# Optimization experiments

Hardware: AMD Instinct MI355X
Metric: run time of the kernel (lower is better)

The kernel has to match this reference:

```python
import jax, jax.numpy as jnp
import numpy as np

B, S, H, D = 4, 2048, 8, 64  # batch, seq, heads, per-head dim (dim=64)
EPS = 1e-5


def _layernorm(h, g, b):
    m = jnp.mean(h, axis=-1, keepdims=True)
    v = jnp.mean(jnp.square(h - m), axis=-1, keepdims=True)
    return (h - m) * jax.lax.rsqrt(v + EPS) * g + b


def setup_inputs() -> dict:
    key = jax.random.key(0)
    ks = jax.random.split(key, 12)
    s = 1.0 / np.sqrt(D)
    return {
        "x": jax.random.normal(ks[0], (B, S, H, D), dtype=jnp.float32),
        "ln1_g": jnp.ones((D,), jnp.float32),
        "ln1_b": jnp.zeros((D,), jnp.float32),
        "Wp": jax.random.normal(ks[1], (D, 3 * D), jnp.float32) * s,
        "bp": jnp.zeros((3 * D,), jnp.float32),
        "ln2_g": jnp.ones((D,), jnp.float32),
        "ln2_b": jnp.zeros((D,), jnp.float32),
        "W1": jax.random.normal(ks[2], (D, 4 * D), jnp.float32) * s,
        "b1": jnp.zeros((4 * D,), jnp.float32),
        "W2": jax.random.normal(ks[3], (4 * D, D), jnp.float32) * (1.0 / np.sqrt(4 * D)),
        "b2": jnp.zeros((D,), jnp.float32),
    }


def reference(x, ln1_g, ln1_b, Wp, bp, ln2_g, ln2_b, W1, b1, W2, b2):
    # x: [B, S, H, D]
    h = _layernorm(x, ln1_g, ln1_b)
    qkv = h @ Wp + bp                       # [B,S,H,3D]  (dropout = identity, eval)
    q, k, v = jnp.split(qkv, 3, axis=-1)
    q = q.transpose(0, 2, 1, 3)             # [B,H,S,D]
    k = k.transpose(0, 2, 1, 3)
    v = v.transpose(0, 2, 1, 3)
    sim = jnp.einsum('bhqd,bhkd->bhqk', q, k)   # no sqrt(d) scaling (faithful)
    attn = jax.nn.softmax(sim, axis=-1)
    out = jnp.einsum('bhqk,bhkd->bhqd', attn, v).transpose(0, 2, 1, 3)  # [B,S,H,D]
    out = _layernorm(out, ln2_g, ln2_b)
    out = jax.nn.gelu(out @ W1 + b1, approximate=False) @ W2 + b2
    return out + x
```

## Files before the change

### kernel.cpp

```cpp
#include <hip/hip_runtime.h>
#include <hip/hip_bf16.h>
#include <math.h>

#define BB 4
#define SS 2048
#define HH 8
#define DD 64
#define EPSV 1e-5f

typedef __attribute__((ext_vector_type(8))) short short8;
typedef __attribute__((ext_vector_type(4))) float f32x4;
typedef unsigned short ushort_t;
#define MFMA16 __builtin_amdgcn_mfma_f32_16x16x32_bf16

__device__ inline unsigned short f2bf(float f) {
    unsigned u = __builtin_bit_cast(unsigned, f);
    unsigned r = (u + 0x7fffu + ((u >> 16) & 1u)) >> 16;
    return (unsigned short)r;
}
__device__ inline float bf2f(unsigned short h) {
    unsigned u = ((unsigned)h) << 16;
    return __builtin_bit_cast(float, u);
}
__device__ inline unsigned pkbf(float a, float b) {
    __hip_bfloat162 h2 = __float22bfloat162_rn(make_float2(a, b));
    unsigned u;
    __builtin_memcpy(&u, &h2, 4);
    return u;
}

__global__ __launch_bounds__(256) void k0_prep(
    const float* __restrict__ Wp, const float* __restrict__ W1,
    const float* __restrict__ W2, ushort_t* __restrict__ WpTh,
    ushort_t* __restrict__ WpTl, ushort_t* __restrict__ W1T,
    ushort_t* __restrict__ W2T)
{
    int gid = blockIdx.x * 256 + threadIdx.x;
    if (gid < 12288) {
        int n = gid >> 6, k = gid & 63;
        float w = Wp[k * 192 + n];
        ushort_t hi = f2bf(w);
        WpTh[gid] = hi;
        WpTl[gid] = f2bf(w - bf2f(hi));
    }
    {
        int n = gid >> 6, k = gid & 63;
        W1T[gid] = f2bf(W1[k * 256 + n]);
    }
    {
        int n = gid >> 8, k = gid & 255;
        W2T[gid] = f2bf(W2[k * 64 + n]);
    }
}

__global__ __launch_bounds__(256) void k1_ln_qkv(
    const float* __restrict__ x, const float* __restrict__ g1, const float* __restrict__ b1v,
    const ushort_t* __restrict__ WpTh, const ushort_t* __restrict__ WpTl,
    const float* __restrict__ bp,
    float* __restrict__ qws, ushort_t* __restrict__ khws, ushort_t* __restrict__ vtws)
{
    __shared__ __align__(16) ushort_t Hh[64 * 72];
    __shared__ __align__(16) ushort_t Hl[64 * 72];
    __shared__ __align__(16) ushort_t Vt[64 * 72];

    const int tid = threadIdx.x;
    const int wv  = tid >> 6;
    const int lane = tid & 63;
    const int l15 = lane & 15;
    const int g   = lane >> 4;
    const int bh  = blockIdx.x & 31;
    const int sc  = blockIdx.x >> 5;
    const int b   = bh >> 3, hh = bh & 7;
    const int s0  = sc * 64;

    short8 bqh[2], bql[2], bkh[2], bkl[2], bvh[2];
    #pragma unroll
    for (int kh = 0; kh < 2; ++kh) {
        int koff = kh * 32 + g * 8;
        bqh[kh] = *(const short8*)(WpTh + (wv * 16 + l15) * 64 + koff);
        bql[kh] = *(const short8*)(WpTl + (wv * 16 + l15) * 64 + koff);
        bkh[kh] = *(const short8*)(WpTh + (64 + wv * 16 + l15) * 64 + koff);
        bkl[kh] = *(const short8*)(WpTl + (64 + wv * 16 + l15) * 64 + koff);
        bvh[kh] = *(const short8*)(WpTh + (128 + wv * 16 + l15) * 64 + koff);
    }
    const float biasq = bp[wv * 16 + l15];
    const float biask = bp[64 + wv * 16 + l15];
    const float biasv = bp[128 + wv * 16 + l15];

    {
        const int srow = s0 + wv * 16 + l15;
        const float* xr = x + ((size_t)(b * 2048 + srow) * 8 + hh) * 64;
        float hvv[16];
        #pragma unroll
        for (int kh = 0; kh < 2; ++kh) {
            float4 p0 = *(const float4*)(xr + kh * 32 + g * 8);
            float4 p1 = *(const float4*)(xr + kh * 32 + g * 8 + 4);
            hvv[kh*8+0]=p0.x; hvv[kh*8+1]=p0.y; hvv[kh*8+2]=p0.z; hvv[kh*8+3]=p0.w;
            hvv[kh*8+4]=p1.x; hvv[kh*8+5]=p1.y; hvv[kh*8+6]=p1.z; hvv[kh*8+7]=p1.w;
        }
        float s1 = 0.0f;
        #pragma unroll
        for (int i = 0; i < 16; ++i) s1 += hvv[i];
        s1 += __shfl_xor(s1, 16, 64);
        s1 += __shfl_xor(s1, 32, 64);
        float mean = s1 * (1.0f / 64.0f);
        float s2 = 0.0f;
        #pragma unroll
        for (int i = 0; i < 16; ++i) { float d = hvv[i] - mean; s2 += d * d; }
        s2 += __shfl_xor(s2, 16, 64);
        s2 += __shfl_xor(s2, 32, 64);
        float rstd = rsqrtf(s2 * (1.0f / 64.0f) + EPSV);

        #pragma unroll
        for (int kh = 0; kh < 2; ++kh) {
            ushort_t hi[8]; unsigned lo2[4];
            float hf[8];
            #pragma unroll
            for (int j = 0; j < 8; ++j) {
                int dI = kh * 32 + g * 8 + j;
                hf[j] = (hvv[kh*8+j] - mean) * rstd * g1[dI] + b1v[dI];
                hi[j] = f2bf(hf[j]);
            }
            uint4 HHv;
            HHv.x = (unsigned)hi[0] | ((unsigned)hi[1] << 16);
            HHv.y = (unsigned)hi[2] | ((unsigned)hi[3] << 16);
            HHv.z = (unsigned)hi[4] | ((unsigned)hi[5] << 16);
            HHv.w = (unsigned)hi[6] | ((unsigned)hi[7] << 16);
            #pragma unroll
            for (int j = 0; j < 4; ++j)
                lo2[j] = pkbf(hf[2*j] - bf2f(hi[2*j]), hf[2*j+1] - bf2f(hi[2*j+1]));
            uint4 HLv; HLv.x = lo2[0]; HLv.y = lo2[1]; HLv.z = lo2[2]; HLv.w = lo2[3];
            int off = (wv * 16 + l15) * 72 + kh * 32 + g * 8;
            *(uint4*)(&Hh[off]) = HHv;
            *(uint4*)(&Hl[off]) = HLv;
        }
    }
    __syncthreads();

    #pragma unroll
    for (int mt = 0; mt < 4; ++mt) {
        short8 ah[2], al[2];
        int abase = (mt * 16 + l15) * 72 + g * 8;
        ah[0] = *(const short8*)(&Hh[abase]);
        ah[1] = *(const short8*)(&Hh[abase + 32]);
        al[0] = *(const short8*)(&Hl[abase]);
        al[1] = *(const short8*)(&Hl[abase + 32]);

        f32x4 aq = (f32x4){0.f,0.f,0.f,0.f};
        f32x4 ak = (f32x4){0.f,0.f,0.f,0.f};
        f32x4 av = (f32x4){0.f,0.f,0.f,0.f};
        #pragma unroll
        for (int kh = 0; kh < 2; ++kh) {
            aq = MFMA16(ah[kh], bqh[kh], aq, 0, 0, 0);
            aq = MFMA16(al[kh], bqh[kh], aq, 0, 0, 0);
            aq = MFMA16(ah[kh], bql[kh], aq, 0, 0, 0);
            ak = MFMA16(ah[kh], bkh[kh], ak, 0, 0, 0);
            ak = MFMA16(al[kh], bkh[kh], ak, 0, 0, 0);
            ak = MFMA16(ah[kh], bkl[kh], ak, 0, 0, 0);
            av = MFMA16(ah[kh], bvh[kh], av, 0, 0, 0);
        }

        size_t base = ((size_t)bh * 2048 + s0 + mt * 16 + 4 * g) * 64 + wv * 16 + l15;
        #pragma unroll
        for (int r = 0; r < 4; ++r) {
            qws[base + (size_t)r * 64] = aq[r] + biasq;
            khws[base + (size_t)r * 64] = f2bf(ak[r] + biask);
        }
        uint2 vvp;
        vvp.x = pkbf(av[0] + biasv, av[1] + biasv);
        vvp.y = pkbf(av[2] + biasv, av[3] + biasv);
        *(uint2*)(&Vt[(wv * 16 + l15) * 72 + mt * 16 + 4 * g]) = vvp;
    }
    __syncthreads();

    #pragma unroll
    for (int p = 0; p < 2; ++p) {
        int slot = tid + 256 * p;
        int dd = slot >> 3, cc = slot & 7;
        *(uint4*)(vtws + ((size_t)bh * 64 + dd) * 2048 + s0 + cc * 8) =
            *(const uint4*)(&Vt[dd * 72 + cc * 8]);
    }
}

#define LROW 72
#define NKT 32

__global__ __launch_bounds__(256, 2) void k2_attn(
    const float* __restrict__ qws, const ushort_t* __restrict__ khws,
    const ushort_t* __restrict__ vtws, float* __restrict__ ows)
{
    __shared__ __align__(16) ushort_t KhL[2][64 * LROW];
    __shared__ __align__(16) ushort_t VtL[2][64 * LROW];
    __shared__ __align__(16) ushort_t PL[128 * LROW];

    const int tid  = threadIdx.x;
    const int w    = tid >> 6;
    const int lane = tid & 63;
    const int l15  = lane & 15;
    const int g    = lane >> 4;
    const int bh   = blockIdx.x & 31;
    const int qb0  = (blockIdx.x >> 5) * 128;

    const float LOG2E = 1.4426950408889634f;
    short8 qh[2][2], ql[2][2];
    #pragma unroll
    for (int sub = 0; sub < 2; ++sub) {
        const float* qp = qws + ((size_t)bh * SS + qb0 + w * 32 + sub * 16 + l15) * 64;
        #pragma unroll
        for (int kh = 0; kh < 2; ++kh) {
            const float* p = qp + 32 * kh + 8 * g;
            #pragma unroll
            for (int j = 0; j < 8; ++j) {
                float f = p[j] * LOG2E;
                ushort_t hi = f2bf(f);
                qh[sub][kh][j] = (short)hi;
                ql[sub][kh][j] = (short)f2bf(f - bf2f(hi));
            }
        }
    }

    float lrow[2] = {0.0f, 0.0f};
    f32x4 oacc[2][4];
    #pragma unroll
    for (int sub = 0; sub < 2; ++sub)
        #pragma unroll
        for (int dt = 0; dt < 4; ++dt) oacc[sub][dt] = (f32x4){0.f, 0.f, 0.f, 0.f};

    const size_t kbase = (size_t)bh * SS * 64;
    const size_t vbase = (size_t)bh * 64 * 2048;

    uint4 kb[2], vb[2];
    #pragma unroll
    for (int rr = 0; rr < 2; ++rr) {
        int slot = tid + 256 * rr;
        int row = slot >> 3, seg = slot & 7;
        kb[rr] = *(const uint4*)(khws + kbase + (size_t)row * 64 + seg * 8);
        vb[rr] = *(const uint4*)(vtws + vbase + (size_t)row * 2048 + seg * 8);
    }
    #pragma unroll
    for (int rr = 0; rr < 2; ++rr) {
        int slot = tid + 256 * rr;
        int row = slot >> 3, seg = slot & 7;
        *(uint4*)(&KhL[0][row * LROW + seg * 8]) = kb[rr];
        *(uint4*)(&VtL[0][row * LROW + seg * 8]) = vb[rr];
    }

    for (int kt = 0; kt < NKT; ++kt) {
        __syncthreads();
        const int cur = kt & 1;

        if (kt < NKT - 1) {
            #pragma unroll
            for (int rr = 0; rr < 2; ++rr) {
                int slot = tid + 256 * rr;
                int row = slot >> 3, seg = slot & 7;
                kb[rr] = *(const uint4*)(khws + kbase + (size_t)((kt + 1) * 64 + row) * 64 + seg * 8);
                vb[rr] = *(const uint4*)(vtws + vbase + (size_t)row * 2048 + (kt + 1) * 64 + seg * 8);
            }
        }

        #pragma unroll
        for (int nf = 0; nf < 4; ++nf) {
            f32x4 aA = (f32x4){0.f, 0.f, 0.f, 0.f};
            f32x4 aB = (f32x4){0.f, 0.f, 0.f, 0.f};
            #pragma unroll
            for (int kh = 0; kh < 2; ++kh) {
                short8 kah = *(const short8*)(&KhL[cur][(nf * 16 + l15) * LROW + 32 * kh + 8 * g]);
                aA = MFMA16(kah, qh[0][kh], aA, 0, 0, 0);
                aA = MFMA16(kah, ql[0][kh], aA, 0, 0, 0);
                aB = MFMA16(kah, qh[1][kh], aB, 0, 0, 0);
                aB = MFMA16(kah, ql[1][kh], aB, 0, 0, 0);
            }
            {
                float p0 = __builtin_amdgcn_exp2f(aA[0]);
                float p1 = __builtin_amdgcn_exp2f(aA[1]);
                float p2 = __builtin_amdgcn_exp2f(aA[2]);
                float p3 = __builtin_amdgcn_exp2f(aA[3]);
                lrow[0] += (p0 + p1) + (p2 + p3);
                uint2 pk; pk.x = pkbf(p0, p1); pk.y = pkbf(p2, p3);
                *(uint2*)(&PL[(w * 32 + l15) * LROW + nf * 16 + 4 * g]) = pk;
            }
            {
                float p0 = __builtin_amdgcn_exp2f(aB[0]);
                float p1 = __builtin_amdgcn_exp2f(aB[1]);
                float p2 = __builtin_amdgcn_exp2f(aB[2]);
                float p3 = __builtin_amdgcn_exp2f(aB[3]);
                lrow[1] += (p0 + p1) + (p2 + p3);
                uint2 pk; pk.x = pkbf(p0, p1); pk.y = pkbf(p2, p3);
                *(uint2*)(&PL[(w * 32 + 16 + l15) * LROW + nf * 16 + 4 * g]) = pk;
            }
        }

        #pragma unroll
        for (int k2i = 0; k2i < 2; ++k2i) {
            short8 paA = *(const short8*)(&PL[(w * 32 + l15) * LROW + k2i * 32 + 8 * g]);
            short8 paB = *(const short8*)(&PL[(w * 32 + 16 + l15) * LROW + k2i * 32 + 8 * g]);
            #pragma unroll
            for (int dt = 0; dt < 4; ++dt) {
                short8 vbf = *(const short8*)(&VtL[cur][(16 * dt + l15) * LROW + k2i * 32 + 8 * g]);
                oacc[0][dt] = MFMA16(paA, vbf, oacc[0][dt], 0, 0, 0);
                oacc[1][dt] = MFMA16(paB, vbf, oacc[1][dt], 0, 0, 0);
            }
        }

        if (kt < NKT - 1) {
            #pragma unroll
            for (int rr = 0; rr < 2; ++rr) {
                int slot = tid + 256 * rr;
                int row = slot >> 3, seg = slot & 7;
                *(uint4*)(&KhL[cur ^ 1][row * LROW + seg * 8]) = kb[rr];
                *(uint4*)(&VtL[cur ^ 1][row * LROW + seg * 8]) = vb[rr];
            }
        }
    }

    #pragma unroll
    for (int sub = 0; sub < 2; ++sub) {
        float l = lrow[sub];
        l += __shfl_xor(l, 16, 64);
        l += __shfl_xor(l, 32, 64);
        float il = 1.0f / l;
        #pragma unroll
        for (int r = 0; r < 4; ++r) {
            float ilr = __shfl(il, 4 * g + r, 64);
            int row = qb0 + w * 32 + sub * 16 + 4 * g + r;
            #pragma unroll
            for (int dt = 0; dt < 4; ++dt)
                ows[((size_t)bh * SS + row) * 64 + dt * 16 + l15] = oacc[sub][dt][r] * ilr;
        }
    }
}

#define ITERS 4

__global__ __launch_bounds__(256) void k3_ln_mlp(
    const float* __restrict__ ows, const float* __restrict__ x,
    const float* __restrict__ g2, const float* __restrict__ b2v,
    const ushort_t* __restrict__ W1T, const float* __restrict__ b1m,
    const ushort_t* __restrict__ W2T, const float* __restrict__ b2o,
    float* __restrict__ out)
{
    __shared__ __align__(16) ushort_t Hs[16 * 264];
    __shared__ __align__(16) float Rs[4 * 16 * 72];

    const int tid  = threadIdx.x;
    const int wv   = tid >> 6;
    const int lane = tid & 63;
    const int l15  = lane & 15;
    const int g    = lane >> 4;

    short8 w1f[4][2], w2f[4][2];
    float  b1r[4][4];
    #pragma unroll
    for (int t = 0; t < 4; ++t) {
        #pragma unroll
        for (int kh = 0; kh < 2; ++kh) {
            w1f[t][kh] = *(const short8*)(W1T + (wv * 64 + t * 16 + l15) * 64 + kh * 32 + g * 8);
            w2f[t][kh] = *(const short8*)(W2T + (t * 16 + l15) * 256 + wv * 64 + kh * 32 + g * 8);
        }
        #pragma unroll
        for (int r = 0; r < 4; ++r)
            b1r[t][r] = b1m[wv * 64 + t * 16 + 4 * g + r];
    }

    for (int it = 0; it < ITERS; ++it) {
        const int r0 = (blockIdx.x * ITERS + it) * 16;

        const float* orow = ows + (size_t)(r0 + l15) * 64;
        float hvv[16];
        #pragma unroll
        for (int kh = 0; kh < 2; ++kh) {
            float4 p0 = *(const float4*)(orow + kh * 32 + g * 8);
            float4 p1 = *(const float4*)(orow + kh * 32 + g * 8 + 4);
            hvv[kh*8+0]=p0.x; hvv[kh*8+1]=p0.y; hvv[kh*8+2]=p0.z; hvv[kh*8+3]=p0.w;
            hvv[kh*8+4]=p1.x; hvv[kh*8+5]=p1.y; hvv[kh*8+6]=p1.z; hvv[kh*8+7]=p1.w;
        }
        float s1 = 0.0f;
        #pragma unroll
        for (int i = 0; i < 16; ++i) s1 += hvv[i];
        s1 += __shfl_xor(s1, 16, 64);
        s1 += __shfl_xor(s1, 32, 64);
        float mean = s1 * (1.0f / 64.0f);
        float s2 = 0.0f;
        #pragma unroll
        for (int i = 0; i < 16; ++i) { float d = hvv[i] - mean; s2 += d * d; }
        s2 += __shfl_xor(s2, 16, 64);
        s2 += __shfl_xor(s2, 32, 64);
        float rstd = rsqrtf(s2 * (1.0f / 64.0f) + EPSV);

        short8 h2f[2];
        #pragma unroll
        for (int kh = 0; kh < 2; ++kh) {
            float4 ga = *(const float4*)(g2 + kh * 32 + g * 8);
            float4 gb = *(const float4*)(g2 + kh * 32 + g * 8 + 4);
            float4 ba = *(const float4*)(b2v + kh * 32 + g * 8);
            float4 bb = *(const float4*)(b2v + kh * 32 + g * 8 + 4);
            float gg[8] = {ga.x,ga.y,ga.z,ga.w,gb.x,gb.y,gb.z,gb.w};
            float bv[8] = {ba.x,ba.y,ba.z,ba.w,bb.x,bb.y,bb.z,bb.w};
            #pragma unroll
            for (int j = 0; j < 8; ++j)
                h2f[kh][j] = (short)f2bf((hvv[kh*8+j] - mean) * rstd * gg[j] + bv[j]);
        }

        #pragma unroll
        for (int t = 0; t < 4; ++t) {
            f32x4 acc = (f32x4){0.f, 0.f, 0.f, 0.f};
            acc = MFMA16(w1f[t][0], h2f[0], acc, 0, 0, 0);
            acc = MFMA16(w1f[t][1], h2f[1], acc, 0, 0, 0);
            float ge[4];
            #pragma unroll
            for (int r = 0; r < 4; ++r) {
                float v = acc[r] + b1r[t][r];
                ge[r] = 0.5f * v * (1.0f + erff(v * 0.70710678118654752f));
            }
            uint2 pk;
            pk.x = pkbf(ge[0], ge[1]);
            pk.y = pkbf(ge[2], ge[3]);
            *(uint2*)(&Hs[l15 * 264 + wv * 64 + t * 16 + 4 * g]) = pk;
        }

        short8 ha[2];
        ha[0] = *(const short8*)(&Hs[l15 * 264 + wv * 64 + g * 8]);
        ha[1] = *(const short8*)(&Hs[l15 * 264 + wv * 64 + 32 + g * 8]);
        #pragma unroll
        for (int t = 0; t < 4; ++t) {
            f32x4 a2 = (f32x4){0.f, 0.f, 0.f, 0.f};
            a2 = MFMA16(ha[0], w2f[t][0], a2, 0, 0, 0);
            a2 = MFMA16(ha[1], w2f[t][1], a2, 0, 0, 0);
            #pragma unroll
            for (int r = 0; r < 4; ++r)
                Rs[wv * 1152 + (4 * g + r) * 72 + t * 16 + l15] = a2[r];
        }
        __syncthreads();

        {
            int m = tid >> 4, d4 = tid & 15;
            const float* rp = Rs + m * 72 + d4 * 4;
            f32x4 v0 = *(const f32x4*)(rp);
            f32x4 v1 = *(const f32x4*)(rp + 1152);
            f32x4 v2 = *(const f32x4*)(rp + 2304);
            f32x4 v3 = *(const f32x4*)(rp + 3456);
            f32x4 sum = v0 + v1 + v2 + v3;
            int r = r0 + m;
            int bq = r >> 14, hq = (r >> 11) & 7, sq = r & 2047;
            size_t oidx = ((size_t)(bq * 2048 + sq) * 8 + hq) * 64 + d4 * 4;
            float4 xv = *(const float4*)(x + oidx);
            float4 bo = *(const float4*)(b2o + d4 * 4);
            float4 res = make_float4(sum[0] + xv.x + bo.x, sum[1] + xv.y + bo.y,
                                     sum[2] + xv.z + bo.z, sum[3] + xv.w + bo.w);
            *(float4*)(out + oidx) = res;
        }
        __syncthreads();
    }
}

extern "C" void kernel_launch(void* const* d_in, const int* in_sizes, int n_in,
                              void* d_out, int out_size, void* d_ws, size_t ws_size,
                              hipStream_t stream) {
    const float* x     = (const float*)d_in[0];
    const float* ln1_g = (const float*)d_in[1];
    const float* ln1_b = (const float*)d_in[2];
    const float* Wp    = (const float*)d_in[3];
    const float* bp    = (const float*)d_in[4];
    const float* ln2_g = (const float*)d_in[5];
    const float* ln2_b = (const float*)d_in[6];
    const float* W1    = (const float*)d_in[7];
    const float* b1    = (const float*)d_in[8];
    const float* W2    = (const float*)d_in[9];
    const float* b2    = (const float*)d_in[10];
    float* out = (float*)d_out;

    float* ws  = (float*)d_ws;
    float* qws = ws;
    float* ows = ws + 4194304;
    ushort_t* khws = (ushort_t*)(ws + 8388608);
    ushort_t* vtws = khws + 4194304;
    ushort_t* WpTh = vtws + 4194304;
    ushort_t* WpTl = WpTh + 12288;
    ushort_t* W1T  = WpTl + 12288;
    ushort_t* W2T  = W1T + 16384;

    k0_prep<<<dim3(64), dim3(256), 0, stream>>>(Wp, W1, W2, WpTh, WpTl, W1T, W2T);
    k1_ln_qkv<<<dim3(1024), dim3(256), 0, stream>>>(
        x, ln1_g, ln1_b, WpTh, WpTl, bp, qws, khws, vtws);
    k2_attn<<<dim3(512), dim3(256), 0, stream>>>(qws, khws, vtws, ows);
    k3_ln_mlp<<<dim3(BB * HH * SS / 16 / ITERS), dim3(256), 0, stream>>>(
        ows, x, ln2_g, ln2_b, W1T, b1, W2T, b2, out);
}
```

Measured before the change: 187.6 us.

## Give each attention wave 64 query rows and precompute split-bf16 Q in QKV kernel

```diff
diff --git a/kernel.cpp b/kernel.cpp
--- a/kernel.cpp
+++ b/kernel.cpp
@@ -57,7 +57,8 @@
     const float* __restrict__ x, const float* __restrict__ g1, const float* __restrict__ b1v,
     const ushort_t* __restrict__ WpTh, const ushort_t* __restrict__ WpTl,
     const float* __restrict__ bp,
-    float* __restrict__ qws, ushort_t* __restrict__ khws, ushort_t* __restrict__ vtws)
+    ushort_t* __restrict__ qhws, ushort_t* __restrict__ qlws,
+    ushort_t* __restrict__ khws, ushort_t* __restrict__ vtws)
 {
     __shared__ __align__(16) ushort_t Hh[64 * 72];
     __shared__ __align__(16) ushort_t Hl[64 * 72];
@@ -72,6 +73,7 @@
     const int sc  = blockIdx.x >> 5;
     const int b   = bh >> 3, hh = bh & 7;
     const int s0  = sc * 64;
+    const float LOG2E = 1.4426950408889634f;
 
     short8 bqh[2], bql[2], bkh[2], bkl[2], bvh[2];
     #pragma unroll
@@ -163,7 +165,10 @@
         size_t base = ((size_t)bh * 2048 + s0 + mt * 16 + 4 * g) * 64 + wv * 16 + l15;
         #pragma unroll
         for (int r = 0; r < 4; ++r) {
-            qws[base + (size_t)r * 64] = aq[r] + biasq;
+            float q = (aq[r] + biasq) * LOG2E;
+            ushort_t q16 = f2bf(q);
+            qhws[base + (size_t)r * 64] = q16;
+            qlws[base + (size_t)r * 64] = f2bf(q - bf2f(q16));
             khws[base + (size_t)r * 64] = f2bf(ak[r] + biask);
         }
         uint2 vvp;
@@ -185,9 +190,10 @@
 #define LROW 72
 #define NKT 32
 
-__global__ __launch_bounds__(256, 2) void k2_attn(
-    const float* __restrict__ qws, const ushort_t* __restrict__ khws,
-    const ushort_t* __restrict__ vtws, float* __restrict__ ows)
+__global__ __launch_bounds__(128, 1) void k2_attn(
+    const ushort_t* __restrict__ qhws, const ushort_t* __restrict__ qlws,
+    const ushort_t* __restrict__ khws, const ushort_t* __restrict__ vtws,
+    float* __restrict__ ows)
 {
     __shared__ __align__(16) ushort_t KhL[2][64 * LROW];
     __shared__ __align__(16) ushort_t VtL[2][64 * LROW];
@@ -201,45 +207,38 @@
     const int bh   = blockIdx.x & 31;
     const int qb0  = (blockIdx.x >> 5) * 128;
 
-    const float LOG2E = 1.4426950408889634f;
-    short8 qh[2][2], ql[2][2];
-    #pragma unroll
-    for (int sub = 0; sub < 2; ++sub) {
-        const float* qp = qws + ((size_t)bh * SS + qb0 + w * 32 + sub * 16 + l15) * 64;
-        #pragma unroll
-        for (int kh = 0; kh < 2; ++kh) {
-            const float* p = qp + 32 * kh + 8 * g;
-            #pragma unroll
-            for (int j = 0; j < 8; ++j) {
-                float f = p[j] * LOG2E;
-                ushort_t hi = f2bf(f);
-                qh[sub][kh][j] = (short)hi;
-                ql[sub][kh][j] = (short)f2bf(f - bf2f(hi));
-            }
-        }
-    }
-
-    float lrow[2] = {0.0f, 0.0f};
-    f32x4 oacc[2][4];
-    #pragma unroll
-    for (int sub = 0; sub < 2; ++sub)
+    short8 qh[4][2], ql[4][2];
+    #pragma unroll
+    for (int sub = 0; sub < 4; ++sub) {
+        size_t qoff = ((size_t)bh * SS + qb0 + w * 64 + sub * 16 + l15) * 64 + g * 8;
+        #pragma unroll
+        for (int kh = 0; kh < 2; ++kh) {
+            qh[sub][kh] = *(const short8*)(qhws + qoff + 32 * kh);
+            ql[sub][kh] = *(const short8*)(qlws + qoff + 32 * kh);
+        }
+    }
+
+    float lrow[4] = {0.f, 0.f, 0.f, 0.f};
+    f32x4 oacc[4][4];
+    #pragma unroll
+    for (int sub = 0; sub < 4; ++sub)
         #pragma unroll
         for (int dt = 0; dt < 4; ++dt) oacc[sub][dt] = (f32x4){0.f, 0.f, 0.f, 0.f};
 
     const size_t kbase = (size_t)bh * SS * 64;
     const size_t vbase = (size_t)bh * 64 * 2048;
 
-    uint4 kb[2], vb[2];
-    #pragma unroll
-    for (int rr = 0; rr < 2; ++rr) {
-        int slot = tid + 256 * rr;
+    uint4 kb[4], vb[4];
+    #pragma unroll
+    for (int rr = 0; rr < 4; ++rr) {
+        int slot = tid + 128 * rr;
         int row = slot >> 3, seg = slot & 7;
         kb[rr] = *(const uint4*)(khws + kbase + (size_t)row * 64 + seg * 8);
         vb[rr] = *(const uint4*)(vtws + vbase + (size_t)row * 2048 + seg * 8);
     }
     #pragma unroll
-    for (int rr = 0; rr < 2; ++rr) {
-        int slot = tid + 256 * rr;
+    for (int rr = 0; rr < 4; ++rr) {
+        int slot = tid + 128 * rr;
         int row = slot >> 3, seg = slot & 7;
         *(uint4*)(&KhL[0][row * LROW + seg * 8]) = kb[rr];
         *(uint4*)(&VtL[0][row * LROW + seg * 8]) = vb[rr];
@@ -251,8 +250,8 @@
 
         if (kt < NKT - 1) {
             #pragma unroll
-            for (int rr = 0; rr < 2; ++rr) {
-                int slot = tid + 256 * rr;
+            for (int rr = 0; rr < 4; ++rr) {
+                int slot = tid + 128 * rr;
                 int row = slot >> 3, seg = slot & 7;
                 kb[rr] = *(const uint4*)(khws + kbase + (size_t)((kt + 1) * 64 + row) * 64 + seg * 8);
                 vb[rr] = *(const uint4*)(vtws + vbase + (size_t)row * 2048 + (kt + 1) * 64 + seg * 8);
@@ -261,52 +260,49 @@
 
         #pragma unroll
         for (int nf = 0; nf < 4; ++nf) {
-            f32x4 aA = (f32x4){0.f, 0.f, 0.f, 0.f};
-            f32x4 aB = (f32x4){0.f, 0.f, 0.f, 0.f};
+            f32x4 aS[4];
+            #pragma unroll
+            for (int sub = 0; sub < 4; ++sub) aS[sub] = (f32x4){0.f, 0.f, 0.f, 0.f};
             #pragma unroll
             for (int kh = 0; kh < 2; ++kh) {
                 short8 kah = *(const short8*)(&KhL[cur][(nf * 16 + l15) * LROW + 32 * kh + 8 * g]);
-                aA = MFMA16(kah, qh[0][kh], aA, 0, 0, 0);
-                aA = MFMA16(kah, ql[0][kh], aA, 0, 0, 0);
-                aB = MFMA16(kah, qh[1][kh], aB, 0, 0, 0);
-                aB = MFMA16(kah, ql[1][kh], aB, 0, 0, 0);
-            }
-            {
-                float p0 = __builtin_amdgcn_exp2f(aA[0]);
-                float p1 = __builtin_amdgcn_exp2f(aA[1]);
-                float p2 = __builtin_amdgcn_exp2f(aA[2]);
-                float p3 = __builtin_amdgcn_exp2f(aA[3]);
-                lrow[0] += (p0 + p1) + (p2 + p3);
+                #pragma unroll
+                for (int sub = 0; sub < 4; ++sub) {
+                    aS[sub] = MFMA16(kah, qh[sub][kh], aS[sub], 0, 0, 0);
+                    aS[sub] = MFMA16(kah, ql[sub][kh], aS[sub], 0, 0, 0);
+                }
+            }
+            #pragma unroll
+            for (int sub = 0; sub < 4; ++sub) {
+                float p0 = __builtin_amdgcn_exp2f(aS[sub][0]);
+                float p1 = __builtin_amdgcn_exp2f(aS[sub][1]);
+                float p2 = __builtin_amdgcn_exp2f(aS[sub][2]);
+                float p3 = __builtin_amdgcn_exp2f(aS[sub][3]);
+                lrow[sub] += (p0 + p1) + (p2 + p3);
                 uint2 pk; pk.x = pkbf(p0, p1); pk.y = pkbf(p2, p3);
-                *(uint2*)(&PL[(w * 32 + l15) * LROW + nf * 16 + 4 * g]) = pk;
-            }
-            {
-                float p0 = __builtin_amdgcn_exp2f(aB[0]);
-                float p1 = __builtin_amdgcn_exp2f(aB[1]);
-                float p2 = __builtin_amdgcn_exp2f(aB[2]);
-                float p3 = __builtin_amdgcn_exp2f(aB[3]);
-                lrow[1] += (p0 + p1) + (p2 + p3);
-                uint2 pk; pk.x = pkbf(p0, p1); pk.y = pkbf(p2, p3);
-                *(uint2*)(&PL[(w * 32 + 16 + l15) * LROW + nf * 16 + 4 * g]) = pk;
+                *(uint2*)(&PL[(w * 64 + sub * 16 + l15) * LROW + nf * 16 + 4 * g]) = pk;
             }
         }
 
         #pragma unroll
         for (int k2i = 0; k2i < 2; ++k2i) {
-            short8 paA = *(const short8*)(&PL[(w * 32 + l15) * LROW + k2i * 32 + 8 * g]);
-            short8 paB = *(const short8*)(&PL[(w * 32 + 16 + l15) * LROW + k2i * 32 + 8 * g]);
+            short8 pa[4];
+            #pragma unroll
+            for (int sub = 0; sub < 4; ++sub)
+                pa[sub] = *(const short8*)(&PL[(w * 64 + sub * 16 + l15) * LROW + k2i * 32 + 8 * g]);
             #pragma unroll
             for (int dt = 0; dt < 4; ++dt) {
                 short8 vbf = *(const short8*)(&VtL[cur][(16 * dt + l15) * LROW + k2i * 32 + 8 * g]);
-                oacc[0][dt] = MFMA16(paA, vbf, oacc[0][dt], 0, 0, 0);
-                oacc[1][dt] = MFMA16(paB, vbf, oacc[1][dt], 0, 0, 0);
+                #pragma unroll
+                for (int sub = 0; sub < 4; ++sub)
+                    oacc[sub][dt] = MFMA16(pa[sub], vbf, oacc[sub][dt], 0, 0, 0);
             }
         }
 
         if (kt < NKT - 1) {
             #pragma unroll
-            for (int rr = 0; rr < 2; ++rr) {
-                int slot = tid + 256 * rr;
+            for (int rr = 0; rr < 4; ++rr) {
+                int slot = tid + 128 * rr;
                 int row = slot >> 3, seg = slot & 7;
                 *(uint4*)(&KhL[cur ^ 1][row * LROW + seg * 8]) = kb[rr];
                 *(uint4*)(&VtL[cur ^ 1][row * LROW + seg * 8]) = vb[rr];
@@ -315,7 +311,7 @@
     }
 
     #pragma unroll
-    for (int sub = 0; sub < 2; ++sub) {
+    for (int sub = 0; sub < 4; ++sub) {
         float l = lrow[sub];
         l += __shfl_xor(l, 16, 64);
         l += __shfl_xor(l, 32, 64);
@@ -323,7 +319,7 @@
         #pragma unroll
         for (int r = 0; r < 4; ++r) {
             float ilr = __shfl(il, 4 * g + r, 64);
-            int row = qb0 + w * 32 + sub * 16 + 4 * g + r;
+            int row = qb0 + w * 64 + sub * 16 + 4 * g + r;
             #pragma unroll
             for (int dt = 0; dt < 4; ++dt)
                 ows[((size_t)bh * SS + row) * 64 + dt * 16 + l15] = oacc[sub][dt][r] * ilr;
@@ -471,9 +467,10 @@
     float* out = (float*)d_out;
 
     float* ws  = (float*)d_ws;
-    float* qws = ws;
-    float* ows = ws + 4194304;
-    ushort_t* khws = (ushort_t*)(ws + 8388608);
+    float* ows = ws;
+    ushort_t* qhws = (ushort_t*)(ws + 4194304);
+    ushort_t* qlws = qhws + 4194304;
+    ushort_t* khws = qlws + 4194304;
     ushort_t* vtws = khws + 4194304;
     ushort_t* WpTh = vtws + 4194304;
     ushort_t* WpTl = WpTh + 12288;
@@ -482,8 +479,8 @@
 
     k0_prep<<<dim3(64), dim3(256), 0, stream>>>(Wp, W1, W2, WpTh, WpTl, W1T, W2T);
     k1_ln_qkv<<<dim3(1024), dim3(256), 0, stream>>>(
-        x, ln1_g, ln1_b, WpTh, WpTl, bp, qws, khws, vtws);
-    k2_attn<<<dim3(512), dim3(256), 0, stream>>>(qws, khws, vtws, ows);
+        x, ln1_g, ln1_b, WpTh, WpTl, bp, qhws, qlws, khws, vtws);
+    k2_attn<<<dim3(512), dim3(128), 0, stream>>>(qhws, qlws, khws, vtws, ows);
     k3_ln_mlp<<<dim3(BB * HH * SS / 16 / ITERS), dim3(256), 0, stream>>>(
         ows, x, ln2_g, ln2_b, W1T, b1, W2T, b2, out);
 }
```

After: 263.4 us. +40.4%, slower.
